# Kernel optimization log

Measured on AMD Instinct MI355X. Metric: run time of the kernel, lower is better.

## Reference

```python
import jax, jax.numpy as jnp
import numpy as np

_BN = 1.0 / np.sqrt(1.0 + 1e-5)  # eval-mode BatchNorm1d with default (fresh-init) stats/affine

def bn(z):
    return z * _BN

def lrelu(z, a):
    return jnp.where(z >= 0, z, a * z)

NEG = -9e15

def setup_inputs() -> dict:
    key = jax.random.key(0)
    ks = jax.random.split(key, 20)
    H = Wd = 256; B = 200; N = 2048; NHID = 128; OUT = 64; HEADS = 4
    x = jax.random.normal(ks[0], (H, Wd, B), dtype=jnp.float32)
    Q = jax.random.uniform(ks[1], (H * Wd, N), dtype=jnp.float32)
    adj = (jax.random.uniform(ks[2], (N, N)) < 0.02).astype(jnp.float32)
    adj = jnp.maximum(adj, jnp.eye(N, dtype=jnp.float32))  # self loops so no empty rows
    def u(k, shape, fan):
        s = 1.0 / np.sqrt(fan)
        return jax.random.uniform(k, shape, jnp.float32, -s, s)
    inp = dict(x=x, adj=adj, Q=Q)
    inp['g1a_W'] = u(ks[3], (B, NHID), NHID);  inp['g1a_b'] = u(ks[4], (NHID,), NHID)
    inp['g1b_W'] = u(ks[5], (NHID, B), B);     inp['g1b_b'] = u(ks[6], (B,), B)
    inp['g2a_W'] = u(ks[7], (B, NHID), NHID);  inp['g2a_b'] = u(ks[8], (NHID,), NHID)
    inp['g2b_W'] = u(ks[9], (NHID, OUT), OUT); inp['g2b_b'] = u(ks[10], (OUT,), OUT)
    inp['gat_W'] = jax.random.normal(ks[11], (HEADS, B, NHID)) * 0.1
    inp['gat_a'] = jax.random.normal(ks[12], (HEADS, 2 * NHID)) * 0.1
    inp['out_W'] = jax.random.normal(ks[13], (HEADS * NHID, OUT)) * 0.1
    inp['out_a'] = jax.random.normal(ks[14], (2 * OUT,)) * 0.1
    inp['Wf'] = u(ks[15], (2, OUT), OUT)
    inp['bf'] = u(ks[16], (2, OUT), OUT)
    inp['conv_w'] = jax.random.normal(ks[17], (3,)) * 0.5
    inp['conv_b'] = jax.random.normal(ks[18], (1,)) * 0.1
    return inp

def reference(x, adj, Q, g1a_W, g1a_b, g1b_W, g1b_b, g2a_W, g2a_b, g2b_W, g2b_b,
              gat_W, gat_a, out_W, out_a, Wf, bf, conv_w, conv_b):
    HW = x.shape[0] * x.shape[1]
    xf = x.reshape(HW, -1)                                   # [HW, C]
    normQ = Q / jnp.sum(Q, axis=0, keepdims=True)            # column-normalized assignment
    sp = normQ.T @ xf                                        # [N, C] superpixel features
    xn = bn(sp)

    # ---- Res_GCN branch ----
    def gcn_block(z, Wa, ba, Wb, bb):
        z = bn(z)
        z = lrelu(adj @ (z @ Wa) + ba, 0.01)
        z = bn(z)
        return adj @ (z @ Wb) + bb

    xg = bn(xn)
    y = lrelu(bn(gcn_block(xg, g1a_W, g1a_b, g1b_W, g1b_b)), 0.01)
    xg = xg + y
    GCN_x = lrelu(bn(gcn_block(xg, g2a_W, g2a_b, g2b_W, g2b_b)), 0.01)  # [N, OUT]

    # ---- GAT branch (fused pairwise scores: e_ij = lrelu(a1.Wh_i + a2.Wh_j)) ----
    mask = adj > 0
    nhid = gat_W.shape[2]

    def gat_head(Wk, ak):
        Wh = xn @ Wk                                         # [N, nhid]
        f1 = Wh @ ak[:nhid]                                  # [N]
        f2 = Wh @ ak[nhid:]                                  # [N]
        e = lrelu(f1[:, None] + f2[None, :], 0.2)            # [N, N]
        att = jax.nn.softmax(jnp.where(mask, e, NEG), axis=1)
        return jax.nn.elu(att @ Wh)                          # concat=True -> ELU

    heads = jax.vmap(gat_head)(gat_W, gat_a)                 # [H, N, nhid]
    hcat = jnp.moveaxis(heads, 0, 1).reshape(heads.shape[1], -1)  # [N, H*nhid]

    fo = out_W.shape[1]
    Wh = hcat @ out_W                                        # [N, OUT]
    e = lrelu((Wh @ out_a[:fo])[:, None] + (Wh @ out_a[fo:])[None, :], 0.2)
    att = jax.nn.softmax(jnp.where(mask, e, NEG), axis=1)
    GAT_x = lrelu(bn(jax.nn.elu(att @ Wh)), 0.01)            # [N, OUT]

    # ---- adaptive fusion ----
    mn = jnp.minimum(GCN_x, GAT_x)
    mx = jnp.maximum(GCN_x, GAT_x)
    avg = (GCN_x * Wf[0] + bf[0]) + (GAT_x * Wf[1] + bf[1])
    stk = jnp.stack([mn, mx, avg], axis=0)                   # [3, N, OUT]
    inp3 = stk + GAT_x + GCN_x                               # broadcast add
    y = jnp.einsum('c,cnf->nf', conv_w, inp3) + conv_b       # 1x1 conv 3->1 channels
    y = lrelu(bn(y), 0.2)                                    # AF2GNN1 leakyrelu(alpha)
    return Q @ y                                             # [HW, OUT]
```

## Files before the change

### kernel.cpp

```cpp
#include <hip/hip_runtime.h>
#include <math.h>

#define BNF 0.9999950000374997f

constexpr int N    = 2048;
constexpr int C    = 200;
constexpr int HW   = 65536;
constexpr int MAXDEG = 96;

typedef unsigned short u16;
typedef __attribute__((ext_vector_type(8))) short short8;
typedef __attribute__((ext_vector_type(4))) float f32x4;

union Frag  { short8 v; ushort4 h[2]; };
union FragA { short8 v; uint2 u2[2]; };

__device__ inline u16 f2bf(float x) {
    unsigned int u = __float_as_uint(x);
    unsigned int r = (u + 0x7fffu + ((u >> 16) & 1u)) >> 16;
    return (u16)r;
}

__device__ __forceinline__ void gload16(const void* g, void* l) {
    __builtin_amdgcn_global_load_lds(
        (const __attribute__((address_space(1))) unsigned int*)g,
        (__attribute__((address_space(3))) unsigned int*)l, 16, 0, 0);
}

__global__ __launch_bounds__(256) void k_convX(const float* __restrict__ xf,
                                               u16* __restrict__ xfT) {
    __shared__ __align__(16) u16 T2[200][140];
    const int i0 = blockIdx.x * 128;
    const int t = threadIdx.x;
    for (int p = 0; p < 25; ++p) {
        int idx = p * 256 + t;
        int il = idx / 50, cq = idx % 50;
        float4 v = *(const float4*)&xf[(size_t)(i0 + il) * 200 + cq * 4];
        T2[cq * 4 + 0][il] = f2bf(v.x);
        T2[cq * 4 + 1][il] = f2bf(v.y);
        T2[cq * 4 + 2][il] = f2bf(v.z);
        T2[cq * 4 + 3][il] = f2bf(v.w);
    }
    __syncthreads();
    for (int p = 0; p < 13; ++p) {
        int c = p * 16 + (t >> 4);
        if (c < 200) {
            int io = (t & 15) * 8;
            u16* dst = &xfT[(size_t)c * 65536 + i0 + io];
            *(ushort4*)&dst[0] = *(const ushort4*)&T2[c][io];
            *(ushort4*)&dst[4] = *(const ushort4*)&T2[c][io + 4];
        }
    }
    ushort4 z4 = {0, 0, 0, 0};
    for (int idx = t; idx < 8 * 16; idx += 256) {
        int r = 200 + (idx >> 4), io = (idx & 15) * 8;
        u16* dst = &xfT[(size_t)r * 65536 + i0 + io];
        *(ushort4*)&dst[0] = z4;
        *(ushort4*)&dst[4] = z4;
    }
}

__global__ __launch_bounds__(256, 3) void k_bigS(const float* __restrict__ Q,
                                                 const u16* __restrict__ xfT,
                                                 u16* __restrict__ Qbf,
                                                 float* __restrict__ S_part,
                                                 float* __restrict__ csPart) {
// ... 117 lines not shown
#undef WRITE_A
#undef LOAD_A
#undef ISSUE_B

    __syncthreads();
    float* csF = (float*)At;
#pragma unroll
    for (int jj = 0; jj < 4; ++jj)
        csF[kp * 64 + nq * 4 + jj] = csum[jj];
    __syncthreads();
    if (t < 64) {
        float s = 0.f;
#pragma unroll
        for (int g2 = 0; g2 < 16; ++g2) s += csF[g2 * 64 + t];
        csPart[(size_t)ks_b * 2048 + n0 + t] = s;
    }
    float* Sp = S_part + (size_t)ks_b * 409600;
#pragma unroll
    for (int nt = 0; nt < 4; ++nt)
#pragma unroll
        for (int c = 0; c < 4; ++c) {
            if (c < nct) {
                const int cc = (ct0 + c) * 16 + (l & 15);
                if (cc < 200) {
                    const int nbase = n0 + nt * 16 + ((l >> 4) << 2);
#pragma unroll
                    for (int r = 0; r < 4; ++r)
                        Sp[(size_t)(nbase + r) * 200 + cc] = acc[nt][c][r];
                }
            }
        }
}

__global__ void k_aux(const float* __restrict__ S_part, const float* __restrict__ csPart,
                      float* __restrict__ xn, float* __restrict__ xg,
                      const float* __restrict__ adj, int* __restrict__ deg,
                      int* __restrict__ idxs) {
    const int bid = blockIdx.x;
    if (bid < 1600) {
        int i = bid * 256 + threadIdx.x;
        if (i >= N * C) return;
        int n = i / C;
        float s = 0.f, csn = 0.f;
#pragma unroll 8
        for (int p = 0; p < 32; ++p) s += S_part[(size_t)p * 409600 + i];
#pragma unroll 8
        for (int p = 0; p < 32; ++p) csn += csPart[(size_t)p * 2048 + n];
        float v = BNF * s / csn;
        xn[i] = v;
        xg[i] = BNF * v;
    } else {
        int w = threadIdx.x >> 6, lane = threadIdx.x & 63;
        int n = (bid - 1600) * 4 + w;
        const float* row = adj + (size_t)n * N;
        int base = 0;
        for (int c = 0; c < N; c += 64) {
            float v = row[c + lane];
            bool p = v > 0.f;
            unsigned long long m = __ballot(p);
            int pos = __popcll(m & ((1ull << lane) - 1ull));
            if (p && (base + pos) < MAXDEG) idxs[(size_t)n * MAXDEG + base + pos] = c + lane;
            base += __popcll(m);
        }
        if (lane == 0) deg[n] = base < MAXDEG ? base : MAXDEG;
    }
}

__global__ __launch_bounds__(256) void k_mm(const float* __restrict__ A,
                                            const float* __restrict__ W,
                                            float* __restrict__ Cc,
                                            int K, int Wout, int ostride,
                                            int zc_off, int zw_str, float scale) {
    __shared__ float ldsA[32][33];
    __shared__ float ldsW[32][64];
    const int rt = blockIdx.x * 32;
    const int ct = blockIdx.y * 64;
    const int z  = blockIdx.z;
    const float* Wp = W + (size_t)z * zw_str;
    const int coff = z * zc_off;
    const int t = threadIdx.x;
    const int lane = t & 63, wg = t >> 6;
    float acc[8];
#pragma unroll
    for (int r = 0; r < 8; ++r) acc[r] = 0.f;

    for (int k0 = 0; k0 < K; k0 += 32) {
        for (int idx = t; idx < 32 * 32; idx += 256) {
            int r = idx >> 5, kk = idx & 31;
            int k = k0 + kk;
            ldsA[r][kk] = (k < K) ? A[(size_t)(rt + r) * K + k] : 0.f;
        }
        for (int idx = t; idx < 32 * 64; idx += 256) {
            int kk = idx >> 6, c = idx & 63;
            int k = k0 + kk, cg = ct + c;
            ldsW[kk][c] = (k < K && cg < Wout) ? Wp[(size_t)k * Wout + cg] : 0.f;
        }
        __syncthreads();
#pragma unroll 8
        for (int kk = 0; kk < 32; ++kk) {
            float wv = ldsW[kk][lane];
#pragma unroll
            for (int r = 0; r < 8; ++r) acc[r] += ldsA[wg * 8 + r][kk] * wv;
        }
        __syncthreads();
    }
    int cg = ct + lane;
    if (cg < Wout) {
#pragma unroll
        for (int r = 0; r < 8; ++r)
            Cc[(size_t)(rt + wg * 8 + r) * ostride + coff + cg] = scale * acc[r];
    }
}

__global__ void k_spmm(const float* __restrict__ h, const int* __restrict__ deg,
                       const int* __restrict__ idxs, const float* __restrict__ bias,
                       const float* __restrict__ res, float* __restrict__ out,
                       int W, float s, int act) {
    int n = blockIdx.x;
    int d = deg[n];
    const int* row = idxs + (size_t)n * MAXDEG;
    int k0 = threadIdx.x;
    int k1 = threadIdx.x + 128;
    float a0 = 0.f, a1 = 0.f;
    for (int j = 0; j < d; ++j) {
        const float* hr = h + (size_t)row[j] * W;
        a0 += hr[k0];
        if (k1 < W) a1 += hr[k1];
    }
    {
        float v = s * (a0 + bias[k0]);
        if (act) v = v >= 0.f ? v : 0.01f * v;
        if (res) v += res[(size_t)n * W + k0];
        out[(size_t)n * W + k0] = v;
    }
    if (k1 < W) {
        float v = s * (a1 + bias[k1]);
        if (act) v = v >= 0.f ? v : 0.01f * v;
        if (res) v += res[(size_t)n * W + k1];
        out[(size_t)n * W + k1] = v;
    }
}

__global__ __launch_bounds__(256) void k_wh5(const float* __restrict__ xn,
                                             const float* __restrict__ gatW,
                                             const float* __restrict__ gata,
                                             const float* __restrict__ g1aW,
                                             float* __restrict__ WhB,
                                             float* __restrict__ f1,
                                             float* __restrict__ f2,
                                             float* __restrict__ hbuf) {
    __shared__ float ldsA[32][33];
    __shared__ float ldsW[32][128];
    __shared__ float ldsWh[32][129];
    const int rt = blockIdx.x * 32;
    const int z  = blockIdx.y;
    const bool gat = z < 4;
    const float* Wp = gat ? gatW + (size_t)z * 25600 : g1aW;
    const int t = threadIdx.x;
    const int col = t & 127, rg = t >> 7;
    float acc[16];
#pragma unroll
    for (int r = 0; r < 16; ++r) acc[r] = 0.f;

    for (int k0 = 0; k0 < 200; k0 += 32) {
        for (int idx = t; idx < 32 * 32; idx += 256) {
            int r = idx >> 5, kk = idx & 31;
            int k = k0 + kk;
            ldsA[r][kk] = (k < 200) ? xn[(size_t)(rt + r) * 200 + k] : 0.f;
        }
        for (int idx = t; idx < 32 * 128; idx += 256) {
            int kk = idx >> 7, c = idx & 127;
            int k = k0 + kk;
            ldsW[kk][c] = (k < 200) ? Wp[(size_t)k * 128 + c] : 0.f;
        }
        __syncthreads();
#pragma unroll 8
        for (int kk = 0; kk < 32; ++kk) {
            float wv = ldsW[kk][col];
#pragma unroll
            for (int r = 0; r < 16; ++r) acc[r] += ldsA[rg * 16 + r][kk] * wv;
        }
        __syncthreads();
    }
    if (gat) {
#pragma unroll
        for (int r = 0; r < 16; ++r) {
            ldsWh[rg * 16 + r][col] = acc[r];
            WhB[(size_t)(rt + rg * 16 + r) * 512 + z * 128 + col] = acc[r];
        }
        __syncthreads();
        int row = t >> 3, p = t & 7;
        const float* a = gata + z * 256;
        float s1 = 0.f, s2 = 0.f;
#pragma unroll
        for (int j = 0; j < 16; ++j) {
            int c = p * 16 + j;
            float v = ldsWh[row][c];
            s1 += v * a[c]; s2 += v * a[128 + c];
        }
        s1 += __shfl_xor(s1, 1); s1 += __shfl_xor(s1, 2); s1 += __shfl_xor(s1, 4);
        s2 += __shfl_xor(s2, 1); s2 += __shfl_xor(s2, 2); s2 += __shfl_xor(s2, 4);
        if (p == 0) { f1[z * N + rt + row] = s1; f2[z * N + rt + row] = s2; }
    } else {
        const float sc = BNF * BNF;
#pragma unroll
        for (int r = 0; r < 16; ++r)
            hbuf[(size_t)(rt + rg * 16 + r) * 128 + col] = sc * acc[r];
    }
}

__global__ void k_att_head(const float* __restrict__ WhB, const float* __restrict__ f1,
                           const float* __restrict__ f2, const int* __restrict__ deg,
                           const int* __restrict__ idxs, float* __restrict__ hcat) {
    __shared__ float eW[MAXDEG];
    int n = blockIdx.x, h = blockIdx.y;
    int k = threadIdx.x;
    int d = deg[n];
    const int* row = idxs + (size_t)n * MAXDEG;
    float f1v = f1[h * N + n];
    const float* f2h = f2 + h * N;
    if (k < d) {
        float e = f1v + f2h[row[k]];
        eW[k] = e >= 0.f ? e : 0.2f * e;
    }
    __syncthreads();
    float mx = -1e30f;
    for (int j = 0; j < d; ++j) mx = fmaxf(mx, eW[j]);
    __syncthreads();
    if (k < d) eW[k] = __expf(eW[k] - mx);
    __syncthreads();
    float ssum = 0.f, acc = 0.f;
    for (int j = 0; j < d; ++j) ssum += eW[j];
    for (int j = 0; j < d; ++j)
        acc += eW[j] * WhB[(size_t)row[j] * 512 + h * 128 + k];
    float v = acc / ssum;
    v = v > 0.f ? v : __expf(v) - 1.f;
    hcat[(size_t)n * 512 + h * 128 + k] = v;
}

__global__ __launch_bounds__(256) void k_mmO(const float* __restrict__ hcat,
                                             const float* __restrict__ outW,
                                             const float* __restrict__ outa,
                                             float* __restrict__ WhO,
                                             float* __restrict__ f1o,
                                             float* __restrict__ f2o) {
    __shared__ float ldsA[32][33];
    __shared__ float ldsW[32][64];
    const int rt = blockIdx.x * 32;
    const int t = threadIdx.x;
    const int lane = t & 63, wg = t >> 6;
    float acc[8];
#pragma unroll
    for (int r = 0; r < 8; ++r) acc[r] = 0.f;

    for (int k0 = 0; k0 < 512; k0 += 32) {
        for (int idx = t; idx < 32 * 32; idx += 256) {
            int r = idx >> 5, kk = idx & 31;
            ldsA[r][kk] = hcat[(size_t)(rt + r) * 512 + k0 + kk];
        }
        for (int idx = t; idx < 32 * 64; idx += 256) {
            int kk = idx >> 6, c = idx & 63;
            ldsW[kk][c] = outW[(size_t)(k0 + kk) * 64 + c];
        }
        __syncthreads();
#pragma unroll 8
        for (int kk = 0; kk < 32; ++kk) {
            float wv = ldsW[kk][lane];
#pragma unroll
            for (int r = 0; r < 8; ++r) acc[r] += ldsA[wg * 8 + r][kk] * wv;
        }
        __syncthreads();
    }
#pragma unroll
    for (int r = 0; r < 8; ++r)
        WhO[(size_t)(rt + wg * 8 + r) * 64 + lane] = acc[r];
#pragma unroll
    for (int r = 0; r < 8; ++r) {
        float v1 = acc[r] * outa[lane];
        float v2 = acc[r] * outa[64 + lane];
#pragma unroll
        for (int off = 32; off; off >>= 1) {
            v1 += __shfl_down(v1, off);
            v2 += __shfl_down(v2, off);
        }
        if (lane == 0) { f1o[rt + wg * 8 + r] = v1; f2o[rt + wg * 8 + r] = v2; }
    }
}

__global__ void k_att_out(const float* __restrict__ WhO, const float* __restrict__ f1o,
                          const float* __restrict__ f2o, const int* __restrict__ deg,
                          const int* __restrict__ idxs, const float* __restrict__ GCNx,
                          const float* __restrict__ Wf, const float* __restrict__ bfp,
                          const float* __restrict__ cw, const float* __restrict__ cb,
                          u16* __restrict__ yT) {
    __shared__ float eW[MAXDEG];
    int n = blockIdx.x;
    int k = threadIdx.x;
    int d = deg[n];
    const int* row = idxs + (size_t)n * MAXDEG;
    float f1v = f1o[n];
    for (int j = k; j < d; j += 64) {
        float e = f1v + f2o[row[j]];
        eW[j] = e >= 0.f ? e : 0.2f * e;
    }
    __syncthreads();
    float mx = -1e30f;
    for (int j = 0; j < d; ++j) mx = fmaxf(mx, eW[j]);
    __syncthreads();
    for (int j = k; j < d; j += 64) eW[j] = __expf(eW[j] - mx);
    __syncthreads();
    float ssum = 0.f, acc = 0.f;
    for (int j = 0; j < d; ++j) ssum += eW[j];
    for (int j = 0; j < d; ++j)
        acc += eW[j] * WhO[(size_t)row[j] * 64 + k];
    float v = acc / ssum;
    v = v > 0.f ? v : __expf(v) - 1.f;
    v *= BNF;
    float gat = v >= 0.f ? v : 0.01f * v;
    float g = GCNx[(size_t)n * 64 + k];
    float mn = fminf(g, gat), mxv = fmaxf(g, gat);
    float avg = g * Wf[k] + bfp[k] + gat * Wf[64 + k] + bfp[64 + k];
    float base = g + gat;
    float yv = cw[0] * (mn + base) + cw[1] * (mxv + base) + cw[2] * (avg + base) + cb[0];
    yv *= BNF;
    yv = yv >= 0.f ? yv : 0.2f * yv;
    yT[k * 2048 + n] = f2bf(yv);
}

__global__ __launch_bounds__(256, 2) void k_final(const u16* __restrict__ Qbf,
                                                  const u16* __restrict__ yT,
                                                  float* __restrict__ out) {
    __shared__ __align__(16) u16 Aq[3][128 * 64];
    __shared__ __align__(16) u16 By[3][64 * 64];
    const int i0 = blockIdx.x * 128;
    const int t = threadIdx.x, w = t >> 6, l = t & 63;
    const int lrow = l >> 3;
    const int scol = (((l & 7) ^ ((l >> 3) & 7)) << 3);
    f32x4 acc[2][4];
#pragma unroll
    for (int a = 0; a < 2; ++a)
#pragma unroll
        for (int b = 0; b < 4; ++b) acc[a][b] = (f32x4){0.f, 0.f, 0.f, 0.f};

#define STAGE_F(buf, step)                                                          \
    {                                                                               \
        const size_t kc = (size_t)(step) * 64 + scol;                               \
        for (int s = w; s < 16; s += 4)                                             \
            gload16(&Qbf[(size_t)(i0 + s * 8 + lrow) * 2048 + kc],                  \
                    &Aq[buf][s * 512]);                                             \
        for (int s = w; s < 8; s += 4)                                              \
            gload16(&yT[(size_t)(s * 8 + lrow) * 2048 + kc],                        \
                    &By[buf][s * 512]);                                             \
    }

    STAGE_F(0, 0);
    STAGE_F(1, 1);
    for (int step = 0; step < 32; ++step) {
        const int cur = step % 3;
        if (step + 2 < 32) STAGE_F((step + 2) % 3, step + 2);
// ... 35 lines not shown
            const int i = i0 + w * 32 + it * 16 + ((l >> 4) << 2);
            const int f = ft * 16 + (l & 15);
#pragma unroll
            for (int r = 0; r < 4; ++r)
                out[(size_t)(i + r) * 64 + f] = acc[it][ft][r];
        }
}

extern "C" void kernel_launch(void* const* d_in, const int* in_sizes, int n_in,
                              void* d_out, int out_size, void* d_ws, size_t ws_size,
                              hipStream_t stream) {
    const float* x     = (const float*)d_in[0];
    const float* adj   = (const float*)d_in[1];
    const float* Q     = (const float*)d_in[2];
    const float* g1aW  = (const float*)d_in[3];
    const float* g1ab  = (const float*)d_in[4];
    const float* g1bW  = (const float*)d_in[5];
    const float* g1bb  = (const float*)d_in[6];
    const float* g2aW  = (const float*)d_in[7];
    const float* g2ab  = (const float*)d_in[8];
    const float* g2bW  = (const float*)d_in[9];
    const float* g2bb  = (const float*)d_in[10];
    const float* gatW  = (const float*)d_in[11];
    const float* gata  = (const float*)d_in[12];
    const float* outW  = (const float*)d_in[13];
    const float* outa  = (const float*)d_in[14];
    const float* Wf    = (const float*)d_in[15];
    const float* bfp   = (const float*)d_in[16];
    const float* convw = (const float*)d_in[17];
    const float* convb = (const float*)d_in[18];

    float* ws   = (float*)d_ws;
    float* xn   = ws + 411648;
    float* xg   = ws + 821248;
    float* xg2  = ws + 1230848;
    float* hbuf = ws + 1640448;
    float* zbuf = ws + 2050048;
    float* WhO  = ws + 2312192;
    float* GCNx = ws + 2443264;
    float* f1   = ws + 2836480;
    float* f2   = ws + 2844672;
    float* f1o  = ws + 2852864;
    float* f2o  = ws + 2854912;
    int*   deg  = (int*)(ws + 2856960);
    int*   idxs = (int*)(ws + 2859008);
    u16*   yT   = (u16*)(ws + 1640448);
    float* csPart = ws + 3000000;
    float* S_part = ws + 4200000;
    u16*   Qbf    = (u16*)(ws + 71308864);
    u16*   xfT    = (u16*)(ws + 138417728);

    float* out  = (float*)d_out;
    float* WhB  = out;
    float* hcat = out + 1048576;

    k_convX<<<512, 256, 0, stream>>>(x, xfT);
    k_bigS<<<1024, 256, 0, stream>>>(Q, xfT, Qbf, S_part, csPart);
    k_aux<<<2112, 256, 0, stream>>>(S_part, csPart, xn, xg, adj, deg, idxs);

    k_wh5<<<dim3(64, 5), 256, 0, stream>>>(xn, gatW, gata, g1aW, WhB, f1, f2, hbuf);

    k_spmm<<<N, 128, 0, stream>>>(hbuf, deg, idxs, g1ab, nullptr, zbuf, 128, 1.f, 1);
    k_att_head<<<dim3(N, 4), 128, 0, stream>>>(WhB, f1, f2, deg, idxs, hcat);
    k_mm<<<dim3(64, 4, 1), 256, 0, stream>>>(zbuf, g1bW, hbuf, 128, 200, 200, 0, 0, BNF);
    k_mmO<<<64, 256, 0, stream>>>(hcat, outW, outa, WhO, f1o, f2o);
    k_spmm<<<N, 128, 0, stream>>>(hbuf, deg, idxs, g1bb, xg, xg2, 200, BNF, 1);
    k_mm<<<dim3(64, 2, 1), 256, 0, stream>>>(xg2, g2aW, hbuf, 200, 128, 128, 0, 0, BNF);
    k_spmm<<<N, 128, 0, stream>>>(hbuf, deg, idxs, g2ab, nullptr, zbuf, 128, 1.f, 1);
    k_mm<<<dim3(64, 1, 1), 256, 0, stream>>>(zbuf, g2bW, hbuf, 128, 64, 64, 0, 0, BNF);
    k_spmm<<<N, 64, 0, stream>>>(hbuf, deg, idxs, g2bb, nullptr, GCNx, 64, BNF, 1);

    k_att_out<<<N, 64, 0, stream>>>(WhO, f1o, f2o, deg, idxs, GCNx,
                                    Wf, bfp, convw, convb, yT);

    k_final<<<512, 256, 0, stream>>>(Qbf, yT, out);
}
```

Baseline: 694.5 us.

## Fuse mid-pipeline GCN/GAT kernels into one cooperative persistent kernel

Replaces the chain of about a dozen small kernels (aux reduction, adjacency compaction, projection GEMMs, SpMMs, attention heads, output attention and fusion) with a single cooperative kernel of 512 blocks. The stages are separated by grid-wide syncs, and blocks loop over virtual block indices. The aim is to remove per-kernel launch overhead and the gaps between launches for these small, latency-bound stages. The cost is about ten grid barriers, fixed-size work mapping and a 256-thread block shape for every stage. It also drops the separate xg buffer by scaling xn inline as the residual.

```diff
diff --git a/kernel.cpp b/kernel.cpp
--- a/kernel.cpp
+++ b/kernel.cpp
@@ -1,5 +1,8 @@
 #include <hip/hip_runtime.h>
+#include <hip/hip_cooperative_groups.h>
 #include <math.h>
+
+namespace cg = cooperative_groups;
 
 #define BNF 0.9999950000374997f
 
@@ -7,6 +10,7 @@
 constexpr int C    = 200;
 constexpr int HW   = 65536;
 constexpr int MAXDEG = 96;
+constexpr int GRID = 512;
 
 typedef unsigned short u16;
 typedef __attribute__((ext_vector_type(8))) short short8;
@@ -215,75 +219,63 @@
         }
 }
 
-__global__ void k_aux(const float* __restrict__ S_part, const float* __restrict__ csPart,
-                      float* __restrict__ xn, float* __restrict__ xg,
-                      const float* __restrict__ adj, int* __restrict__ deg,
-                      int* __restrict__ idxs) {
-    const int bid = blockIdx.x;
-    if (bid < 1600) {
-        int i = bid * 256 + threadIdx.x;
-        if (i >= N * C) return;
-        int n = i / C;
-        float s = 0.f, csn = 0.f;
-#pragma unroll 8
-        for (int p = 0; p < 32; ++p) s += S_part[(size_t)p * 409600 + i];
-#pragma unroll 8
-        for (int p = 0; p < 32; ++p) csn += csPart[(size_t)p * 2048 + n];
-        float v = BNF * s / csn;
-        xn[i] = v;
-        xg[i] = BNF * v;
-    } else {
-        int w = threadIdx.x >> 6, lane = threadIdx.x & 63;
-        int n = (bid - 1600) * 4 + w;
-        const float* row = adj + (size_t)n * N;
-        int base = 0;
-        for (int c = 0; c < N; c += 64) {
-            float v = row[c + lane];
-            bool p = v > 0.f;
-            unsigned long long m = __ballot(p);
-            int pos = __popcll(m & ((1ull << lane) - 1ull));
-            if (p && (base + pos) < MAXDEG) idxs[(size_t)n * MAXDEG + base + pos] = c + lane;
-            base += __popcll(m);
-        }
-        if (lane == 0) deg[n] = base < MAXDEG ? base : MAXDEG;
-    }
-}
-
-__global__ __launch_bounds__(256) void k_mm(const float* __restrict__ A,
-                                            const float* __restrict__ W,
-                                            float* __restrict__ Cc,
-                                            int K, int Wout, int ostride,
-                                            int zc_off, int zw_str, float scale) {
-    __shared__ float ldsA[32][33];
-    __shared__ float ldsW[32][64];
-    const int rt = blockIdx.x * 32;
-    const int ct = blockIdx.y * 64;
-    const int z  = blockIdx.z;
-    const float* Wp = W + (size_t)z * zw_str;
-    const int coff = z * zc_off;
-    const int t = threadIdx.x;
+struct MegaArgs {
+    const float* S_part; const float* csPart; float* xn;
+    const float* adj; int* deg; int* idxs;
+    const float* gatW; const float* gata; const float* g1aW;
+    float* WhB; float* f1; float* f2; float* hbuf;
+    const float* g1ab; float* zbuf;
+    float* hcat;
+    const float* g1bW;
+    const float* outW; const float* outa; float* WhO; float* f1o; float* f2o;
+    const float* g1bb; float* xg2;
+    const float* g2aW; const float* g2ab; const float* g2bW; const float* g2bb;
+    float* GCNx;
+    const float* Wf; const float* bfp; const float* cw; const float* cb;
+    u16* yT;
+};
+
+__device__ inline void spmm_body(int n, int k, int W, const float* h,
+                                 const int* deg, const int* idxs,
+                                 const float* bias, const float* res, float rs,
+                                 float* out, float s) {
+    if (k < W) {
+        int d = deg[n];
+        const int* row = idxs + (size_t)n * MAXDEG;
+        float a = 0.f;
+        for (int j = 0; j < d; ++j) a += h[(size_t)row[j] * W + k];
+        float v = s * (a + bias[k]);
+        v = v >= 0.f ? v : 0.01f * v;
+        if (res) v += rs * res[(size_t)n * W + k];
+        out[(size_t)n * W + k] = v;
+    }
+}
+
+__device__ inline void mm_dev(const float* Ag, const float* Wp, float* Cc,
+                              int K, int Wout, int ostride, float scale,
+                              int rt, int ct, int t,
+                              float (&lA)[32][33], float (&lW)[32][129]) {
     const int lane = t & 63, wg = t >> 6;
     float acc[8];
 #pragma unroll
     for (int r = 0; r < 8; ++r) acc[r] = 0.f;
-
     for (int k0 = 0; k0 < K; k0 += 32) {
-        for (int idx = t; idx < 32 * 32; idx += 256) {
+        for (int idx = t; idx < 1024; idx += 256) {
             int r = idx >> 5, kk = idx & 31;
             int k = k0 + kk;
-            ldsA[r][kk] = (k < K) ? A[(size_t)(rt + r) * K + k] : 0.f;
-        }
-        for (int idx = t; idx < 32 * 64; idx += 256) {
+            lA[r][kk] = (k < K) ? Ag[(size_t)(rt + r) * K + k] : 0.f;
+        }
+        for (int idx = t; idx < 2048; idx += 256) {
             int kk = idx >> 6, c = idx & 63;
             int k = k0 + kk, cg = ct + c;
-            ldsW[kk][c] = (k < K && cg < Wout) ? Wp[(size_t)k * Wout + cg] : 0.f;
+            lW[kk][c] = (k < K && cg < Wout) ? Wp[(size_t)k * Wout + cg] : 0.f;
         }
         __syncthreads();
 #pragma unroll 8
         for (int kk = 0; kk < 32; ++kk) {
-            float wv = ldsW[kk][lane];
-#pragma unroll
-            for (int r = 0; r < 8; ++r) acc[r] += ldsA[wg * 8 + r][kk] * wv;
+            float wv = lW[kk][lane];
+#pragma unroll
+            for (int r = 0; r < 8; ++r) acc[r] += lA[wg * 8 + r][kk] * wv;
         }
         __syncthreads();
     }
@@ -291,223 +283,252 @@
     if (cg < Wout) {
 #pragma unroll
         for (int r = 0; r < 8; ++r)
-            Cc[(size_t)(rt + wg * 8 + r) * ostride + coff + cg] = scale * acc[r];
-    }
-}
-
-__global__ void k_spmm(const float* __restrict__ h, const int* __restrict__ deg,
-                       const int* __restrict__ idxs, const float* __restrict__ bias,
-                       const float* __restrict__ res, float* __restrict__ out,
-                       int W, float s, int act) {
-    int n = blockIdx.x;
-    int d = deg[n];
-    const int* row = idxs + (size_t)n * MAXDEG;
-    int k0 = threadIdx.x;
-    int k1 = threadIdx.x + 128;
-    float a0 = 0.f, a1 = 0.f;
-    for (int j = 0; j < d; ++j) {
-        const float* hr = h + (size_t)row[j] * W;
-        a0 += hr[k0];
-        if (k1 < W) a1 += hr[k1];
-    }
-    {
-        float v = s * (a0 + bias[k0]);
-        if (act) v = v >= 0.f ? v : 0.01f * v;
-        if (res) v += res[(size_t)n * W + k0];
-        out[(size_t)n * W + k0] = v;
-    }
-    if (k1 < W) {
-        float v = s * (a1 + bias[k1]);
-        if (act) v = v >= 0.f ? v : 0.01f * v;
-        if (res) v += res[(size_t)n * W + k1];
-        out[(size_t)n * W + k1] = v;
-    }
-}
-
-__global__ __launch_bounds__(256) void k_wh5(const float* __restrict__ xn,
-                                             const float* __restrict__ gatW,
-                                             const float* __restrict__ gata,
-                                             const float* __restrict__ g1aW,
-                                             float* __restrict__ WhB,
-                                             float* __restrict__ f1,
-                                             float* __restrict__ f2,
-                                             float* __restrict__ hbuf) {
+            Cc[(size_t)(rt + wg * 8 + r) * ostride + cg] = scale * acc[r];
+    }
+}
+
+__global__ __launch_bounds__(256, 2) void k_mega(MegaArgs A) {
+    cg::grid_group grid = cg::this_grid();
+    const int bid = blockIdx.x;
+    const int t = threadIdx.x;
+
     __shared__ float ldsA[32][33];
-    __shared__ float ldsW[32][128];
+    __shared__ float ldsW[32][129];
     __shared__ float ldsWh[32][129];
-    const int rt = blockIdx.x * 32;
-    const int z  = blockIdx.y;
-    const bool gat = z < 4;
-    const float* Wp = gat ? gatW + (size_t)z * 25600 : g1aW;
-    const int t = threadIdx.x;
-    const int col = t & 127, rg = t >> 7;
-    float acc[16];
-#pragma unroll
-    for (int r = 0; r < 16; ++r) acc[r] = 0.f;
-
-    for (int k0 = 0; k0 < 200; k0 += 32) {
-        for (int idx = t; idx < 32 * 32; idx += 256) {
-            int r = idx >> 5, kk = idx & 31;
-            int k = k0 + kk;
-            ldsA[r][kk] = (k < 200) ? xn[(size_t)(rt + r) * 200 + k] : 0.f;
-        }
-        for (int idx = t; idx < 32 * 128; idx += 256) {
-            int kk = idx >> 7, c = idx & 127;
-            int k = k0 + kk;
-            ldsW[kk][c] = (k < 200) ? Wp[(size_t)k * 128 + c] : 0.f;
+    __shared__ float eW[512];
+
+    for (int vb = bid; vb < 2112; vb += GRID) {
+        if (vb < 1600) {
+            int i = vb * 256 + t;
+            if (i < N * C) {
+                int n = i / C;
+                float s = 0.f, csn = 0.f;
+#pragma unroll 8
+                for (int p = 0; p < 32; ++p) s += A.S_part[(size_t)p * 409600 + i];
+#pragma unroll 8
+                for (int p = 0; p < 32; ++p) csn += A.csPart[(size_t)p * 2048 + n];
+                A.xn[i] = BNF * s / csn;
+            }
+        } else {
+            int w = t >> 6, lane = t & 63;
+            int n = (vb - 1600) * 4 + w;
+            const float* row = A.adj + (size_t)n * N;
+            int base = 0;
+            for (int c = 0; c < N; c += 64) {
+                float v = row[c + lane];
+                bool p = v > 0.f;
+                unsigned long long m = __ballot(p);
+                int pos = __popcll(m & ((1ull << lane) - 1ull));
+                if (p && (base + pos) < MAXDEG)
+                    A.idxs[(size_t)n * MAXDEG + base + pos] = c + lane;
+                base += __popcll(m);
+            }
+            if (lane == 0) A.deg[n] = base < MAXDEG ? base : MAXDEG;
+        }
+    }
+    __threadfence(); grid.sync();
+
+    for (int vb = bid; vb < 320; vb += GRID) {
+        const int rt = (vb & 63) * 32;
+        const int z  = vb >> 6;
+        const bool gat = z < 4;
+        const float* Wp = gat ? A.gatW + (size_t)z * 25600 : A.g1aW;
+        const int col = t & 127, rg = t >> 7;
+        float acc[16];
+#pragma unroll
+        for (int r = 0; r < 16; ++r) acc[r] = 0.f;
+        for (int k0 = 0; k0 < 200; k0 += 32) {
+            for (int idx = t; idx < 1024; idx += 256) {
+                int r = idx >> 5, kk = idx & 31;
+                int k = k0 + kk;
+                ldsA[r][kk] = (k < 200) ? A.xn[(size_t)(rt + r) * 200 + k] : 0.f;
+            }
+            for (int idx = t; idx < 4096; idx += 256) {
+                int kk = idx >> 7, c = idx & 127;
+                int k = k0 + kk;
+                ldsW[kk][c] = (k < 200) ? Wp[(size_t)k * 128 + c] : 0.f;
+            }
+            __syncthreads();
+#pragma unroll 8
+            for (int kk = 0; kk < 32; ++kk) {
+                float wv = ldsW[kk][col];
+#pragma unroll
+                for (int r = 0; r < 16; ++r) acc[r] += ldsA[rg * 16 + r][kk] * wv;
+            }
+            __syncthreads();
+        }
+        if (gat) {
+#pragma unroll
+            for (int r = 0; r < 16; ++r) {
+                ldsWh[rg * 16 + r][col] = acc[r];
+                A.WhB[(size_t)(rt + rg * 16 + r) * 512 + z * 128 + col] = acc[r];
+            }
+            __syncthreads();
+            int row = t >> 3, p = t & 7;
+            const float* a = A.gata + z * 256;
+            float s1 = 0.f, s2 = 0.f;
+#pragma unroll
+            for (int j = 0; j < 16; ++j) {
+                int c = p * 16 + j;
+                float v = ldsWh[row][c];
+                s1 += v * a[c]; s2 += v * a[128 + c];
+            }
+            s1 += __shfl_xor(s1, 1); s1 += __shfl_xor(s1, 2); s1 += __shfl_xor(s1, 4);
+            s2 += __shfl_xor(s2, 1); s2 += __shfl_xor(s2, 2); s2 += __shfl_xor(s2, 4);
+            if (p == 0) { A.f1[z * N + rt + row] = s1; A.f2[z * N + rt + row] = s2; }
+            __syncthreads();
+        } else {
+            const float sc = BNF * BNF;
+#pragma unroll
+            for (int r = 0; r < 16; ++r)
+                A.hbuf[(size_t)(rt + rg * 16 + r) * 128 + col] = sc * acc[r];
+        }
+    }
+    __threadfence(); grid.sync();
+
+    for (int vb = bid; vb < 5120; vb += GRID) {
+        if (vb < 1024) {
+            int n = vb * 2 + (t >> 7);
+            spmm_body(n, t & 127, 128, A.hbuf, A.deg, A.idxs, A.g1ab,
+                      nullptr, 0.f, A.zbuf, 1.f);
+        } else {
+            const int va = vb - 1024;
+            const int half = t >> 7, k = t & 127;
+            const int u = va * 2 + half;
+            const int h = u >> 11, n = u & 2047;
+            const int d = A.deg[n];
+            const int* row = A.idxs + (size_t)n * MAXDEG;
+            const float f1v = A.f1[h * N + n];
+            const float* f2h = A.f2 + h * N;
+            float* e = eW + half * 128;
+            if (k < d) {
+                float ev = f1v + f2h[row[k]];
+                e[k] = ev >= 0.f ? ev : 0.2f * ev;
+            }
+            __syncthreads();
+            float mx = -1e30f;
+            for (int j = 0; j < d; ++j) mx = fmaxf(mx, e[j]);
+            __syncthreads();
+            if (k < d) e[k] = __expf(e[k] - mx);
+            __syncthreads();
+            float ssum = 0.f, acc = 0.f;
+            for (int j = 0; j < d; ++j) ssum += e[j];
+            for (int j = 0; j < d; ++j)
+                acc += e[j] * A.WhB[(size_t)row[j] * 512 + h * 128 + k];
+            float v = acc / ssum;
+            v = v > 0.f ? v : __expf(v) - 1.f;
+            A.hcat[(size_t)n * 512 + h * 128 + k] = v;
+            __syncthreads();
+        }
+    }
+    __threadfence(); grid.sync();
+
+    for (int vb = bid; vb < 320; vb += GRID) {
+        if (vb < 256) {
+            mm_dev(A.zbuf, A.g1bW, A.hbuf, 128, 200, 200, BNF,
+                   (vb & 63) * 32, (vb >> 6) * 64, t, ldsA, ldsW);
+        } else {
+            const int rt = (vb - 256) * 32;
+            const int lane = t & 63, wg = t >> 6;
+            float acc[8];
+#pragma unroll
+            for (int r = 0; r < 8; ++r) acc[r] = 0.f;
+            for (int k0 = 0; k0 < 512; k0 += 32) {
+                for (int idx = t; idx < 1024; idx += 256) {
+                    int r = idx >> 5, kk = idx & 31;
+                    ldsA[r][kk] = A.hcat[(size_t)(rt + r) * 512 + k0 + kk];
+                }
+                for (int idx = t; idx < 2048; idx += 256) {
+                    int kk = idx >> 6, c = idx & 63;
+                    ldsW[kk][c] = A.outW[(size_t)(k0 + kk) * 64 + c];
+                }
+                __syncthreads();
+#pragma unroll 8
+                for (int kk = 0; kk < 32; ++kk) {
+                    float wv = ldsW[kk][lane];
+#pragma unroll
+                    for (int r = 0; r < 8; ++r) acc[r] += ldsA[wg * 8 + r][kk] * wv;
+                }
+                __syncthreads();
+            }
+#pragma unroll
+            for (int r = 0; r < 8; ++r)
+                A.WhO[(size_t)(rt + wg * 8 + r) * 64 + lane] = acc[r];
+#pragma unroll
+            for (int r = 0; r < 8; ++r) {
+                float v1 = acc[r] * A.outa[lane];
+                float v2 = acc[r] * A.outa[64 + lane];
+#pragma unroll
+                for (int off = 32; off; off >>= 1) {
+                    v1 += __shfl_down(v1, off);
+                    v2 += __shfl_down(v2, off);
+                }
+                if (lane == 0) { A.f1o[rt + wg * 8 + r] = v1; A.f2o[rt + wg * 8 + r] = v2; }
+            }
+        }
+    }
+    __threadfence(); grid.sync();
+
+    for (int vb = bid; vb < 2048; vb += GRID)
+        spmm_body(vb, t, 200, A.hbuf, A.deg, A.idxs, A.g1bb, A.xn, BNF,
+                  A.xg2, BNF);
+    __threadfence(); grid.sync();
+
+    for (int vb = bid; vb < 128; vb += GRID)
+        mm_dev(A.xg2, A.g2aW, A.hbuf, 200, 128, 128, BNF,
+               (vb & 63) * 32, (vb >> 6) * 64, t, ldsA, ldsW);
+    __threadfence(); grid.sync();
+
+    for (int vb = bid; vb < 1024; vb += GRID)
+        spmm_body(vb * 2 + (t >> 7), t & 127, 128, A.hbuf, A.deg, A.idxs,
+                  A.g2ab, nullptr, 0.f, A.zbuf, 1.f);
+    __threadfence(); grid.sync();
+
+    for (int vb = bid; vb < 64; vb += GRID)
+        mm_dev(A.zbuf, A.g2bW, A.hbuf, 128, 64, 64, BNF, vb * 32, 0, t,
+               ldsA, ldsW);
+    __threadfence(); grid.sync();
+
+    for (int vb = bid; vb < 512; vb += GRID)
+        spmm_body(vb * 4 + (t >> 6), t & 63, 64, A.hbuf, A.deg, A.idxs,
+                  A.g2bb, nullptr, 0.f, A.GCNx, BNF);
+    __threadfence(); grid.sync();
+
+    for (int vb = bid; vb < 512; vb += GRID) {
+        const int sub = t >> 6, k = t & 63;
+        const int n = vb * 4 + sub;
+        const int d = A.deg[n];
+        const int* row = A.idxs + (size_t)n * MAXDEG;
+        const float f1v = A.f1o[n];
+        float* e = eW + sub * 128;
+        for (int j = k; j < d; j += 64) {
+            float ev = f1v + A.f2o[row[j]];
+            e[j] = ev >= 0.f ? ev : 0.2f * ev;
         }
         __syncthreads();
-#pragma unroll 8
-        for (int kk = 0; kk < 32; ++kk) {
-            float wv = ldsW[kk][col];
-#pragma unroll
-            for (int r = 0; r < 16; ++r) acc[r] += ldsA[rg * 16 + r][kk] * wv;
-        }
+        float mx = -1e30f;
+        for (int j = 0; j < d; ++j) mx = fmaxf(mx, e[j]);
         __syncthreads();
-    }
-    if (gat) {
-#pragma unroll
-        for (int r = 0; r < 16; ++r) {
-            ldsWh[rg * 16 + r][col] = acc[r];
-            WhB[(size_t)(rt + rg * 16 + r) * 512 + z * 128 + col] = acc[r];
-        }
+        for (int j = k; j < d; j += 64) e[j] = __expf(e[j] - mx);
         __syncthreads();
-        int row = t >> 3, p = t & 7;
-        const float* a = gata + z * 256;
-        float s1 = 0.f, s2 = 0.f;
-#pragma unroll
-        for (int j = 0; j < 16; ++j) {
-            int c = p * 16 + j;
-            float v = ldsWh[row][c];
-            s1 += v * a[c]; s2 += v * a[128 + c];
-        }
-        s1 += __shfl_xor(s1, 1); s1 += __shfl_xor(s1, 2); s1 += __shfl_xor(s1, 4);
-        s2 += __shfl_xor(s2, 1); s2 += __shfl_xor(s2, 2); s2 += __shfl_xor(s2, 4);
-        if (p == 0) { f1[z * N + rt + row] = s1; f2[z * N + rt + row] = s2; }
-    } else {
-        const float sc = BNF * BNF;
-#pragma unroll
-        for (int r = 0; r < 16; ++r)
-            hbuf[(size_t)(rt + rg * 16 + r) * 128 + col] = sc * acc[r];
-    }
-}
-
-__global__ void k_att_head(const float* __restrict__ WhB, const float* __restrict__ f1,
-                           const float* __restrict__ f2, const int* __restrict__ deg,
-                           const int* __restrict__ idxs, float* __restrict__ hcat) {
-    __shared__ float eW[MAXDEG];
-    int n = blockIdx.x, h = blockIdx.y;
-    int k = threadIdx.x;
-    int d = deg[n];
-    const int* row = idxs + (size_t)n * MAXDEG;
-    float f1v = f1[h * N + n];
-    const float* f2h = f2 + h * N;
-    if (k < d) {
-        float e = f1v + f2h[row[k]];
-        eW[k] = e >= 0.f ? e : 0.2f * e;
-    }
-    __syncthreads();
-    float mx = -1e30f;
-    for (int j = 0; j < d; ++j) mx = fmaxf(mx, eW[j]);
-    __syncthreads();
-    if (k < d) eW[k] = __expf(eW[k] - mx);
-    __syncthreads();
-    float ssum = 0.f, acc = 0.f;
-    for (int j = 0; j < d; ++j) ssum += eW[j];
-    for (int j = 0; j < d; ++j)
-        acc += eW[j] * WhB[(size_t)row[j] * 512 + h * 128 + k];
-    float v = acc / ssum;
-    v = v > 0.f ? v : __expf(v) - 1.f;
-    hcat[(size_t)n * 512 + h * 128 + k] = v;
-}
-
-__global__ __launch_bounds__(256) void k_mmO(const float* __restrict__ hcat,
-                                             const float* __restrict__ outW,
-                                             const float* __restrict__ outa,
-                                             float* __restrict__ WhO,
-                                             float* __restrict__ f1o,
-                                             float* __restrict__ f2o) {
-    __shared__ float ldsA[32][33];
-    __shared__ float ldsW[32][64];
-    const int rt = blockIdx.x * 32;
-    const int t = threadIdx.x;
-    const int lane = t & 63, wg = t >> 6;
-    float acc[8];
-#pragma unroll
-    for (int r = 0; r < 8; ++r) acc[r] = 0.f;
-
-    for (int k0 = 0; k0 < 512; k0 += 32) {
-        for (int idx = t; idx < 32 * 32; idx += 256) {
-            int r = idx >> 5, kk = idx & 31;
-            ldsA[r][kk] = hcat[(size_t)(rt + r) * 512 + k0 + kk];
-        }
-        for (int idx = t; idx < 32 * 64; idx += 256) {
-            int kk = idx >> 6, c = idx & 63;
-            ldsW[kk][c] = outW[(size_t)(k0 + kk) * 64 + c];
-        }
+        float ssum = 0.f, acc = 0.f;
+        for (int j = 0; j < d; ++j) ssum += e[j];
+        for (int j = 0; j < d; ++j) acc += e[j] * A.WhO[(size_t)row[j] * 64 + k];
+        float v = acc / ssum;
+        v = v > 0.f ? v : __expf(v) - 1.f;
+        v *= BNF;
+        float gat = v >= 0.f ? v : 0.01f * v;
+        float g = A.GCNx[(size_t)n * 64 + k];
+        float mn = fminf(g, gat), mxv = fmaxf(g, gat);
+        float avg = g * A.Wf[k] + A.bfp[k] + gat * A.Wf[64 + k] + A.bfp[64 + k];
+        float base = g + gat;
+        float yv = A.cw[0] * (mn + base) + A.cw[1] * (mxv + base)
+                 + A.cw[2] * (avg + base) + A.cb[0];
+        yv *= BNF;
+        yv = yv >= 0.f ? yv : 0.2f * yv;
+        A.yT[k * 2048 + n] = f2bf(yv);
         __syncthreads();
-#pragma unroll 8
-        for (int kk = 0; kk < 32; ++kk) {
-            float wv = ldsW[kk][lane];
-#pragma unroll
-            for (int r = 0; r < 8; ++r) acc[r] += ldsA[wg * 8 + r][kk] * wv;
-        }
-        __syncthreads();
-    }
-#pragma unroll
-    for (int r = 0; r < 8; ++r)
-        WhO[(size_t)(rt + wg * 8 + r) * 64 + lane] = acc[r];
-#pragma unroll
-    for (int r = 0; r < 8; ++r) {
-        float v1 = acc[r] * outa[lane];
-        float v2 = acc[r] * outa[64 + lane];
-#pragma unroll
-        for (int off = 32; off; off >>= 1) {
-            v1 += __shfl_down(v1, off);
-            v2 += __shfl_down(v2, off);
-        }
-        if (lane == 0) { f1o[rt + wg * 8 + r] = v1; f2o[rt + wg * 8 + r] = v2; }
-    }
-}
-
-__global__ void k_att_out(const float* __restrict__ WhO, const float* __restrict__ f1o,
-                          const float* __restrict__ f2o, const int* __restrict__ deg,
-                          const int* __restrict__ idxs, const float* __restrict__ GCNx,
-                          const float* __restrict__ Wf, const float* __restrict__ bfp,
-                          const float* __restrict__ cw, const float* __restrict__ cb,
-                          u16* __restrict__ yT) {
-    __shared__ float eW[MAXDEG];
-    int n = blockIdx.x;
-    int k = threadIdx.x;
-    int d = deg[n];
-    const int* row = idxs + (size_t)n * MAXDEG;
-    float f1v = f1o[n];
-    for (int j = k; j < d; j += 64) {
-        float e = f1v + f2o[row[j]];
-        eW[j] = e >= 0.f ? e : 0.2f * e;
-    }
-    __syncthreads();
-    float mx = -1e30f;
-    for (int j = 0; j < d; ++j) mx = fmaxf(mx, eW[j]);
-    __syncthreads();
-    for (int j = k; j < d; j += 64) eW[j] = __expf(eW[j] - mx);
-    __syncthreads();
-    float ssum = 0.f, acc = 0.f;
-    for (int j = 0; j < d; ++j) ssum += eW[j];
-    for (int j = 0; j < d; ++j)
-        acc += eW[j] * WhO[(size_t)row[j] * 64 + k];
-    float v = acc / ssum;
-    v = v > 0.f ? v : __expf(v) - 1.f;
-    v *= BNF;
-    float gat = v >= 0.f ? v : 0.01f * v;
-    float g = GCNx[(size_t)n * 64 + k];
-    float mn = fminf(g, gat), mxv = fmaxf(g, gat);
-    float avg = g * Wf[k] + bfp[k] + gat * Wf[64 + k] + bfp[64 + k];
-    float base = g + gat;
-    float yv = cw[0] * (mn + base) + cw[1] * (mxv + base) + cw[2] * (avg + base) + cb[0];
-    yv *= BNF;
-    yv = yv >= 0.f ? yv : 0.2f * yv;
-    yT[k * 2048 + n] = f2bf(yv);
+    }
 }
 
 __global__ __launch_bounds__(256, 2) void k_final(const u16* __restrict__ Qbf,
@@ -609,7 +630,6 @@
 
     float* ws   = (float*)d_ws;
     float* xn   = ws + 411648;
-    float* xg   = ws + 821248;
     float* xg2  = ws + 1230848;
     float* hbuf = ws + 1640448;
     float* zbuf = ws + 2050048;
@@ -633,22 +653,23 @@
 
     k_convX<<<512, 256, 0, stream>>>(x, xfT);
     k_bigS<<<1024, 256, 0, stream>>>(Q, xfT, Qbf, S_part, csPart);
-    k_aux<<<2112, 256, 0, stream>>>(S_part, csPart, xn, xg, adj, deg, idxs);
-
-    k_wh5<<<dim3(64, 5), 256, 0, stream>>>(xn, gatW, gata, g1aW, WhB, f1, f2, hbuf);
-
-    k_spmm<<<N, 128, 0, stream>>>(hbuf, deg, idxs, g1ab, nullptr, zbuf, 128, 1.f, 1);
-    k_att_head<<<dim3(N, 4), 128, 0, stream>>>(WhB, f1, f2, deg, idxs, hcat);
-    k_mm<<<dim3(64, 4, 1), 256, 0, stream>>>(zbuf, g1bW, hbuf, 128, 200, 200, 0, 0, BNF);
-    k_mmO<<<64, 256, 0, stream>>>(hcat, outW, outa, WhO, f1o, f2o);
-    k_spmm<<<N, 128, 0, stream>>>(hbuf, deg, idxs, g1bb, xg, xg2, 200, BNF, 1);
-    k_mm<<<dim3(64, 2, 1), 256, 0, stream>>>(xg2, g2aW, hbuf, 200, 128, 128, 0, 0, BNF);
-    k_spmm<<<N, 128, 0, stream>>>(hbuf, deg, idxs, g2ab, nullptr, zbuf, 128, 1.f, 1);
-    k_mm<<<dim3(64, 1, 1), 256, 0, stream>>>(zbuf, g2bW, hbuf, 128, 64, 64, 0, 0, BNF);
-    k_spmm<<<N, 64, 0, stream>>>(hbuf, deg, idxs, g2bb, nullptr, GCNx, 64, BNF, 1);
-
-    k_att_out<<<N, 64, 0, stream>>>(WhO, f1o, f2o, deg, idxs, GCNx,
-                                    Wf, bfp, convw, convb, yT);
+
+    MegaArgs ma;
+    ma.S_part = S_part; ma.csPart = csPart; ma.xn = xn;
+    ma.adj = adj; ma.deg = deg; ma.idxs = idxs;
+    ma.gatW = gatW; ma.gata = gata; ma.g1aW = g1aW;
+    ma.WhB = WhB; ma.f1 = f1; ma.f2 = f2; ma.hbuf = hbuf;
+    ma.g1ab = g1ab; ma.zbuf = zbuf;
+    ma.hcat = hcat;
+    ma.g1bW = g1bW;
+    ma.outW = outW; ma.outa = outa; ma.WhO = WhO; ma.f1o = f1o; ma.f2o = f2o;
+    ma.g1bb = g1bb; ma.xg2 = xg2;
+    ma.g2aW = g2aW; ma.g2ab = g2ab; ma.g2bW = g2bW; ma.g2bb = g2bb;
+    ma.GCNx = GCNx;
+    ma.Wf = Wf; ma.bfp = bfp; ma.cw = convw; ma.cb = convb;
+    ma.yT = yT;
+    void* kargs[] = { &ma };
+    hipLaunchCooperativeKernel((void*)k_mega, dim3(GRID), dim3(256), kargs, 0, stream);
 
     k_final<<<512, 256, 0, stream>>>(Qbf, yT, out);
 }
```

Measured after the change: 1.674 ms. 141% more time.

## Merge independent small kernels into horizontally fused launches to cut launch count

Applied to the files above, without the earlier changes.

Moves the adjacency-to-index-list scan into extra blocks of the transpose kernel. Merges the first GCN sparse aggregation with the GAT head attention into one launch, and the following two dense matmuls into another, with block-index dispatch choosing the work. The goal is to remove launch overhead and tail idle time from several small, independent kernels. The cost is more divergent kernels, higher register and shared-memory pressure, and the csPart buffer moving in the workspace.

```diff
diff --git a/kernel.cpp b/kernel.cpp
--- a/kernel.cpp
+++ b/kernel.cpp
@@ -28,10 +28,30 @@
 }
 
 __global__ __launch_bounds__(256) void k_convX(const float* __restrict__ xf,
-                                               u16* __restrict__ xfT) {
+                                               u16* __restrict__ xfT,
+                                               const float* __restrict__ adj,
+                                               int* __restrict__ deg,
+                                               int* __restrict__ idxs) {
+    const int t = threadIdx.x;
+    if (blockIdx.x >= 512) {
+        int w = t >> 6, lane = t & 63;
+        int n = (blockIdx.x - 512) * 4 + w;
+        const float* row = adj + (size_t)n * N;
+        int base = 0;
+        for (int c = 0; c < N; c += 64) {
+            float v = row[c + lane];
+            bool p = v > 0.f;
+            unsigned long long m = __ballot(p);
+            int pos = __popcll(m & ((1ull << lane) - 1ull));
+            if (p && (base + pos) < MAXDEG)
+                idxs[(size_t)n * MAXDEG + base + pos] = c + lane;
+            base += __popcll(m);
+        }
+        if (lane == 0) deg[n] = base < MAXDEG ? base : MAXDEG;
+        return;
+    }
     __shared__ __align__(16) u16 T2[200][140];
     const int i0 = blockIdx.x * 128;
-    const int t = threadIdx.x;
     for (int p = 0; p < 25; ++p) {
         int idx = p * 256 + t;
         int il = idx / 50, cq = idx % 50;
@@ -215,38 +235,19 @@
         }
 }
 
-__global__ void k_aux(const float* __restrict__ S_part, const float* __restrict__ csPart,
-                      float* __restrict__ xn, float* __restrict__ xg,
-                      const float* __restrict__ adj, int* __restrict__ deg,
-                      int* __restrict__ idxs) {
-    const int bid = blockIdx.x;
-    if (bid < 1600) {
-        int i = bid * 256 + threadIdx.x;
-        if (i >= N * C) return;
-        int n = i / C;
-        float s = 0.f, csn = 0.f;
+__global__ void k_redS(const float* __restrict__ S_part, const float* __restrict__ csPart,
+                       float* __restrict__ xn, float* __restrict__ xg) {
+    int i = blockIdx.x * 256 + threadIdx.x;
+    if (i >= N * C) return;
+    int n = i / C;
+    float s = 0.f, csn = 0.f;
 #pragma unroll 8
-        for (int p = 0; p < 32; ++p) s += S_part[(size_t)p * 409600 + i];
+    for (int p = 0; p < 32; ++p) s += S_part[(size_t)p * 409600 + i];
 #pragma unroll 8
-        for (int p = 0; p < 32; ++p) csn += csPart[(size_t)p * 2048 + n];
-        float v = BNF * s / csn;
-        xn[i] = v;
-        xg[i] = BNF * v;
-    } else {
-        int w = threadIdx.x >> 6, lane = threadIdx.x & 63;
-        int n = (bid - 1600) * 4 + w;
-        const float* row = adj + (size_t)n * N;
-        int base = 0;
-        for (int c = 0; c < N; c += 64) {
-            float v = row[c + lane];
-            bool p = v > 0.f;
-            unsigned long long m = __ballot(p);
-            int pos = __popcll(m & ((1ull << lane) - 1ull));
-            if (p && (base + pos) < MAXDEG) idxs[(size_t)n * MAXDEG + base + pos] = c + lane;
-            base += __popcll(m);
-        }
-        if (lane == 0) deg[n] = base < MAXDEG ? base : MAXDEG;
-    }
+    for (int p = 0; p < 32; ++p) csn += csPart[(size_t)p * 2048 + n];
+    float v = BNF * s / csn;
+    xn[i] = v;
+    xg[i] = BNF * v;
 }
 
 __global__ __launch_bounds__(256) void k_mm(const float* __restrict__ A,
@@ -392,81 +393,132 @@
     }
 }
 
-__global__ void k_att_head(const float* __restrict__ WhB, const float* __restrict__ f1,
-                           const float* __restrict__ f2, const int* __restrict__ deg,
-                           const int* __restrict__ idxs, float* __restrict__ hcat) {
-    __shared__ float eW[MAXDEG];
-    int n = blockIdx.x, h = blockIdx.y;
-    int k = threadIdx.x;
-    int d = deg[n];
-    const int* row = idxs + (size_t)n * MAXDEG;
-    float f1v = f1[h * N + n];
-    const float* f2h = f2 + h * N;
-    if (k < d) {
-        float e = f1v + f2h[row[k]];
-        eW[k] = e >= 0.f ? e : 0.2f * e;
-    }
-    __syncthreads();
-    float mx = -1e30f;
-    for (int j = 0; j < d; ++j) mx = fmaxf(mx, eW[j]);
-    __syncthreads();
-    if (k < d) eW[k] = __expf(eW[k] - mx);
-    __syncthreads();
-    float ssum = 0.f, acc = 0.f;
-    for (int j = 0; j < d; ++j) ssum += eW[j];
-    for (int j = 0; j < d; ++j)
-        acc += eW[j] * WhB[(size_t)row[j] * 512 + h * 128 + k];
-    float v = acc / ssum;
-    v = v > 0.f ? v : __expf(v) - 1.f;
-    hcat[(size_t)n * 512 + h * 128 + k] = v;
-}
-
-__global__ __launch_bounds__(256) void k_mmO(const float* __restrict__ hcat,
-                                             const float* __restrict__ outW,
-                                             const float* __restrict__ outa,
-                                             float* __restrict__ WhO,
-                                             float* __restrict__ f1o,
-                                             float* __restrict__ f2o) {
+__global__ void k_s1ah(const float* __restrict__ hbuf, const int* __restrict__ deg,
+                       const int* __restrict__ idxs, const float* __restrict__ g1ab,
+                       float* __restrict__ zbuf, const float* __restrict__ WhB,
+                       const float* __restrict__ f1, const float* __restrict__ f2,
+                       float* __restrict__ hcat) {
+    __shared__ float eW[256];
+    const int vb = blockIdx.x;
+    const int t = threadIdx.x;
+    if (vb < 1024) {
+        const int n = vb * 2 + (t >> 7), k = t & 127;
+        const int d = deg[n];
+        const int* row = idxs + (size_t)n * MAXDEG;
+        float a = 0.f;
+        for (int j = 0; j < d; ++j) a += hbuf[(size_t)row[j] * 128 + k];
+        float v = a + g1ab[k];
+        v = v >= 0.f ? v : 0.01f * v;
+        zbuf[(size_t)n * 128 + k] = v;
+    } else {
+        const int va = vb - 1024;
+        const int half = t >> 7, k = t & 127;
+        const int u = va * 2 + half;
+        const int h = u >> 11, n = u & 2047;
+        const int d = deg[n];
+        const int* row = idxs + (size_t)n * MAXDEG;
+        const float f1v = f1[h * N + n];
+        const float* f2h = f2 + h * N;
+        float* e = eW + half * 128;
+        if (k < d) {
+            float ev = f1v + f2h[row[k]];
+            e[k] = ev >= 0.f ? ev : 0.2f * ev;
+        }
+        __syncthreads();
+        float mx = -1e30f;
+        for (int j = 0; j < d; ++j) mx = fmaxf(mx, e[j]);
+        __syncthreads();
+        if (k < d) e[k] = __expf(e[k] - mx);
+        __syncthreads();
+        float ssum = 0.f, acc = 0.f;
+        for (int j = 0; j < d; ++j) ssum += e[j];
+        for (int j = 0; j < d; ++j)
+            acc += e[j] * WhB[(size_t)row[j] * 512 + h * 128 + k];
+        float v = acc / ssum;
+        v = v > 0.f ? v : __expf(v) - 1.f;
+        hcat[(size_t)n * 512 + h * 128 + k] = v;
+    }
+}
+
+__global__ __launch_bounds__(256) void k_g1bO(const float* __restrict__ zbuf,
+                                              const float* __restrict__ g1bW,
+                                              float* __restrict__ hbuf,
+                                              const float* __restrict__ hcat,
+                                              const float* __restrict__ outW,
+                                              const float* __restrict__ outa,
+                                              float* __restrict__ WhO,
+                                              float* __restrict__ f1o,
+                                              float* __restrict__ f2o) {
     __shared__ float ldsA[32][33];
-    __shared__ float ldsW[32][64];
-    const int rt = blockIdx.x * 32;
+    __shared__ float ldsW[32][65];
+    const int vb = blockIdx.x;
     const int t = threadIdx.x;
     const int lane = t & 63, wg = t >> 6;
     float acc[8];
 #pragma unroll
     for (int r = 0; r < 8; ++r) acc[r] = 0.f;
 
-    for (int k0 = 0; k0 < 512; k0 += 32) {
-        for (int idx = t; idx < 32 * 32; idx += 256) {
-            int r = idx >> 5, kk = idx & 31;
-            ldsA[r][kk] = hcat[(size_t)(rt + r) * 512 + k0 + kk];
-        }
-        for (int idx = t; idx < 32 * 64; idx += 256) {
-            int kk = idx >> 6, c = idx & 63;
-            ldsW[kk][c] = outW[(size_t)(k0 + kk) * 64 + c];
-        }
-        __syncthreads();
+    if (vb < 256) {
+        const int rt = (vb & 63) * 32, ct = (vb >> 6) * 64;
+        for (int k0 = 0; k0 < 128; k0 += 32) {
+            for (int idx = t; idx < 1024; idx += 256) {
+                int r = idx >> 5, kk = idx & 31;
+                ldsA[r][kk] = zbuf[(size_t)(rt + r) * 128 + k0 + kk];
+            }
+            for (int idx = t; idx < 2048; idx += 256) {
+                int kk = idx >> 6, c = idx & 63;
+                int cg = ct + c;
+                ldsW[kk][c] = (cg < 200) ? g1bW[(size_t)(k0 + kk) * 200 + cg] : 0.f;
+            }
+            __syncthreads();
 #pragma unroll 8
-        for (int kk = 0; kk < 32; ++kk) {
-            float wv = ldsW[kk][lane];
-#pragma unroll
-            for (int r = 0; r < 8; ++r) acc[r] += ldsA[wg * 8 + r][kk] * wv;
-        }
-        __syncthreads();
-    }
-#pragma unroll
-    for (int r = 0; r < 8; ++r)
-        WhO[(size_t)(rt + wg * 8 + r) * 64 + lane] = acc[r];
-#pragma unroll
-    for (int r = 0; r < 8; ++r) {
-        float v1 = acc[r] * outa[lane];
-        float v2 = acc[r] * outa[64 + lane];
-#pragma unroll
-        for (int off = 32; off; off >>= 1) {
-            v1 += __shfl_down(v1, off);
-            v2 += __shfl_down(v2, off);
-        }
-        if (lane == 0) { f1o[rt + wg * 8 + r] = v1; f2o[rt + wg * 8 + r] = v2; }
+            for (int kk = 0; kk < 32; ++kk) {
+                float wv = ldsW[kk][lane];
+#pragma unroll
+                for (int r = 0; r < 8; ++r) acc[r] += ldsA[wg * 8 + r][kk] * wv;
+            }
+            __syncthreads();
+        }
+        int cg = ct + lane;
+        if (cg < 200) {
+#pragma unroll
+            for (int r = 0; r < 8; ++r)
+                hbuf[(size_t)(rt + wg * 8 + r) * 200 + cg] = BNF * acc[r];
+        }
+    } else {
+        const int rt = (vb - 256) * 32;
+        for (int k0 = 0; k0 < 512; k0 += 32) {
+            for (int idx = t; idx < 1024; idx += 256) {
+                int r = idx >> 5, kk = idx & 31;
+                ldsA[r][kk] = hcat[(size_t)(rt + r) * 512 + k0 + kk];
+            }
+            for (int idx = t; idx < 2048; idx += 256) {
+                int kk = idx >> 6, c = idx & 63;
+                ldsW[kk][c] = outW[(size_t)(k0 + kk) * 64 + c];
+            }
+            __syncthreads();
+#pragma unroll 8
+            for (int kk = 0; kk < 32; ++kk) {
+                float wv = ldsW[kk][lane];
+#pragma unroll
+                for (int r = 0; r < 8; ++r) acc[r] += ldsA[wg * 8 + r][kk] * wv;
+            }
+            __syncthreads();
+        }
+#pragma unroll
+        for (int r = 0; r < 8; ++r)
+            WhO[(size_t)(rt + wg * 8 + r) * 64 + lane] = acc[r];
+#pragma unroll
+        for (int r = 0; r < 8; ++r) {
+            float v1 = acc[r] * outa[lane];
+            float v2 = acc[r] * outa[64 + lane];
+#pragma unroll
+            for (int off = 32; off; off >>= 1) {
+                v1 += __shfl_down(v1, off);
+                v2 += __shfl_down(v2, off);
+            }
+            if (lane == 0) { f1o[rt + wg * 8 + r] = v1; f2o[rt + wg * 8 + r] = v2; }
+        }
     }
 }
 
@@ -622,7 +674,7 @@
     int*   deg  = (int*)(ws + 2856960);
     int*   idxs = (int*)(ws + 2859008);
     u16*   yT   = (u16*)(ws + 1640448);
-    float* csPart = ws + 3000000;
+    float* csPart = ws + 3600000;
     float* S_part = ws + 4200000;
     u16*   Qbf    = (u16*)(ws + 71308864);
     u16*   xfT    = (u16*)(ws + 138417728);
@@ -631,16 +683,15 @@
     float* WhB  = out;
     float* hcat = out + 1048576;
 
-    k_convX<<<512, 256, 0, stream>>>(x, xfT);
+    k_convX<<<1024, 256, 0, stream>>>(x, xfT, adj, deg, idxs);
     k_bigS<<<1024, 256, 0, stream>>>(Q, xfT, Qbf, S_part, csPart);
-    k_aux<<<2112, 256, 0, stream>>>(S_part, csPart, xn, xg, adj, deg, idxs);
+    k_redS<<<1600, 256, 0, stream>>>(S_part, csPart, xn, xg);
 
     k_wh5<<<dim3(64, 5), 256, 0, stream>>>(xn, gatW, gata, g1aW, WhB, f1, f2, hbuf);
 
-    k_spmm<<<N, 128, 0, stream>>>(hbuf, deg, idxs, g1ab, nullptr, zbuf, 128, 1.f, 1);
-    k_att_head<<<dim3(N, 4), 128, 0, stream>>>(WhB, f1, f2, deg, idxs, hcat);
-    k_mm<<<dim3(64, 4, 1), 256, 0, stream>>>(zbuf, g1bW, hbuf, 128, 200, 200, 0, 0, BNF);
-    k_mmO<<<64, 256, 0, stream>>>(hcat, outW, outa, WhO, f1o, f2o);
+    k_s1ah<<<5120, 256, 0, stream>>>(hbuf, deg, idxs, g1ab, zbuf, WhB, f1, f2, hcat);
+    k_g1bO<<<320, 256, 0, stream>>>(zbuf, g1bW, hbuf, hcat, outW, outa, WhO, f1o, f2o);
+
     k_spmm<<<N, 128, 0, stream>>>(hbuf, deg, idxs, g1bb, xg, xg2, 200, BNF, 1);
     k_mm<<<dim3(64, 2, 1), 256, 0, stream>>>(xg2, g2aW, hbuf, 200, 128, 128, 0, 0, BNF);
     k_spmm<<<N, 128, 0, stream>>>(hbuf, deg, idxs, g2ab, nullptr, zbuf, 128, 1.f, 1);
```

Result: no change. 683.4 us (-1.6%).
